# Performance work log

Hardware: AMD Instinct MI355X
Metric: run time of the kernel (lower is better)

The kernel has to match this reference:

```python
import jax, jax.numpy as jnp
import numpy as np

NUM_EMBEDDINGS = 512
EMBEDDING_DIM = 128
COMMITMENT = 0.25
DECAY = 0.99
EPS = 1e-05


def setup_inputs() -> dict:
    key = jax.random.key(0)
    k1, k2 = jax.random.split(key)
    z = jax.random.normal(k1, (32, EMBEDDING_DIM, 64, 64), dtype=jnp.float32)
    embedding = jax.random.normal(k2, (EMBEDDING_DIM, NUM_EMBEDDINGS), dtype=jnp.float32)
    cluster_size = jnp.zeros((NUM_EMBEDDINGS,), dtype=jnp.float32)
    embed_avg = embedding  # buffer initialized as a clone of embedding
    return {"z": z, "embedding": embedding, "cluster_size": cluster_size, "embed_avg": embed_avg}


def reference(z, embedding, cluster_size, embed_avg):
    sg = jax.lax.stop_gradient
    D, K = embedding.shape
    B, C, H, W = z.shape
    z_perm = jnp.transpose(z, (0, 2, 3, 1))          # [B,H,W,D]
    flat_z = z_perm.reshape(-1, D)                    # [N,D]

    distances = ((flat_z ** 2).sum(1, keepdims=True)
                 - 2.0 * (flat_z @ embedding)
                 + (embedding ** 2).sum(0)[None, :])  # [N,K]
    idx = jnp.argmin(distances, axis=1)               # [N]

    # gather codes (equivalent to one-hot @ embedding.T, without materializing one-hot)
    quantized = jnp.take(embedding.T, idx, axis=0).reshape(z_perm.shape)  # [B,H,W,D]
    quantized = jnp.transpose(quantized, (0, 3, 1, 2))                    # [B,D,H,W]

    # EMA codebook update (training branch)
    enc_sum = jax.ops.segment_sum(jnp.ones_like(idx, dtype=flat_z.dtype), idx, num_segments=K)  # [K]
    embed_sum = jax.ops.segment_sum(flat_z, idx, num_segments=K).T                              # [D,K]
    new_cluster_size = cluster_size * DECAY + (1.0 - DECAY) * enc_sum
    new_embed_avg = embed_avg * DECAY + (1.0 - DECAY) * embed_sum
    n = jnp.maximum(new_cluster_size.sum(), 1e-05)
    cs = (new_cluster_size + EPS) / (n + K * EPS) * n
    new_embedding = new_embed_avg / cs[None, :]

    e_latent_loss = jnp.mean((sg(quantized) - z) ** 2)
    q_latent_loss = jnp.mean((quantized - sg(z)) ** 2)
    loss = q_latent_loss + COMMITMENT * e_latent_loss

    quantized_out = z + sg(quantized - z)             # straight-through
    encoding_indices = idx.reshape(B, H, W)
    return (quantized_out, loss, encoding_indices, new_embedding, new_cluster_size, new_embed_avg)
```

## Files before the change

### kernel.cpp

```cpp
#include <hip/hip_runtime.h>
#include <hip/hip_bf16.h>
#include <float.h>

typedef _Float16 f16;
typedef __attribute__((ext_vector_type(8))) _Float16 half8;
typedef __attribute__((ext_vector_type(4))) float floatx4;

#define DIM   128
#define HW    4096
#define NPOS  131072
#define K     512
#define ZSTRIDE_B 524288

#define Q_OFF     0
#define LOSS_OFF  16777216
#define IDX_OFF   16777217
#define NEMB_OFF  16908289
#define NCS_OFF   16973825
#define NEA_OFF   16974337

#define WS_LOSS  0
#define WS_E2    2
#define WS_ENC   514
#define WS_ESUM  1026
#define WS_ZERO_COUNT 66562
#define WS_EHI   66564
#define WS_ELO   99332

#define XST 136

__global__ __launch_bounds__(256) void k_prep(const float* __restrict__ emb,
                                              f16* __restrict__ ehiP,
                                              f16* __restrict__ eloP,
                                              float* __restrict__ e2) {
    int lin = blockIdx.x * 256 + threadIdx.x;
    int o = lin >> 9, k = lin & 511;
    int g = k >> 4, r = k & 15;
    half8 hh, ll;
    float s = 0.f;
    #pragma unroll
    for (int j = 0; j < 8; ++j) {
        float v = emb[(o * 8 + j) * K + k];
        f16 h = (f16)v;
        f16 l = (f16)(v - (float)h);
        hh[j] = h; ll[j] = l;
        s = fmaf(v, v, s);
    }
    int base = (g * 4 + (o >> 2)) * 512 + (o & 3) * 128 + r * 8;
    *(half8*)&ehiP[base] = hh;
    *(half8*)&eloP[base] = ll;
    unsafeAtomicAdd(&e2[k], s);
}

__global__ __launch_bounds__(256, 2) void k_assign(const float* __restrict__ z,
                                                   const f16* __restrict__ ehiP,
                                                   const f16* __restrict__ eloP,
                                                   const float* __restrict__ e2,
                                                   float* __restrict__ out,
                                                   float* __restrict__ lossAcc) {
    __shared__ f16 xs_h[64 * XST];
    __shared__ f16 xs_l[64 * XST];
    __shared__ float wbD[256];
    __shared__ int   wbI[256];
    __shared__ int   bidx[64];
    __shared__ float wred[4];

    const int tid  = threadIdx.x;
    const int lane = tid & 63;
    const int wv   = tid >> 6;
    const int n0   = blockIdx.x * 64;
    const int b    = n0 >> 12;
    const int hw0  = n0 & 4095;
    const float* zb = z + b * ZSTRIDE_B + hw0;
    const int l15  = lane & 15;
    const int quad = lane >> 4;

    float sv0[16], sv1[16];
    #pragma unroll
    for (int it = 0; it < 16; ++it) {
        int lin = tid + it * 256;
        int i  = lin & 63;
        int dp = lin >> 6;
        sv0[it] = zb[(2 * dp) * HW + i];
        sv1[it] = zb[(2 * dp + 1) * HW + i];
    }
    #pragma unroll
    for (int it = 0; it < 16; ++it) {
        int lin = tid + it * 256;
        int i  = lin & 63;
        int dp = lin >> 6;
        float v0 = sv0[it], v1 = sv1[it];
        f16 h0 = (f16)v0; f16 l0 = (f16)(v0 - (float)h0);
        f16 h1 = (f16)v1; f16 l1 = (f16)(v1 - (float)h1);
        union { f16 h[2]; unsigned int u; } ph, pl;
        ph.h[0] = h0; ph.h[1] = h1;
        pl.h[0] = l0; pl.h[1] = l1;
        *(unsigned int*)&xs_h[i * XST + 2 * dp] = ph.u;
        *(unsigned int*)&xs_l[i * XST + 2 * dp] = pl.u;
    }
    __syncthreads();

    float bestD[4][4];
    int   bestI[4][4];
    #pragma unroll
    for (int t = 0; t < 4; ++t)
        #pragma unroll
        for (int r = 0; r < 4; ++r) { bestD[t][r] = FLT_MAX; bestI[t][r] = 0x7fffffff; }

    const half8* gh = (const half8*)ehiP;
    const half8* gl = (const half8*)eloP;

    for (int cc = 0; cc < 4; ++cc) {
        floatx4 acc[4][2];
        #pragma unroll
        for (int t = 0; t < 4; ++t)
            #pragma unroll
            for (int nt = 0; nt < 2; ++nt) acc[t][nt] = (floatx4){0.f, 0.f, 0.f, 0.f};

        for (int dc = 0; dc < 4; ++dc) {
            half8 ah[4], al[4];
            #pragma unroll
            for (int t = 0; t < 4; ++t) {
                int off = (t * 16 + l15) * XST + dc * 32 + quad * 8;
                ah[t] = *(const half8*)&xs_h[off];
                al[t] = *(const half8*)&xs_l[off];
            }
            #pragma unroll
            for (int nt = 0; nt < 2; ++nt) {
                int g  = cc * 8 + wv * 2 + nt;
                int bi = (g * 4 + dc) * 64 + lane;
                half8 bh = gh[bi];
                half8 bl = gl[bi];
                #pragma unroll
                for (int t = 0; t < 4; ++t) {
                    acc[t][nt] = __builtin_amdgcn_mfma_f32_16x16x32_f16(ah[t], bh, acc[t][nt], 0, 0, 0);
                    acc[t][nt] = __builtin_amdgcn_mfma_f32_16x16x32_f16(al[t], bh, acc[t][nt], 0, 0, 0);
                    acc[t][nt] = __builtin_amdgcn_mfma_f32_16x16x32_f16(ah[t], bl, acc[t][nt], 0, 0, 0);
                }
            }
        }
        #pragma unroll
        for (int nt = 0; nt < 2; ++nt) {
            int c = cc * 128 + wv * 32 + nt * 16 + l15;
            float ee = e2[c];
            #pragma unroll
            for (int t = 0; t < 4; ++t)
                #pragma unroll
                for (int r = 0; r < 4; ++r) {
                    float s = fmaf(-2.f, acc[t][nt][r], ee);
                    if (s < bestD[t][r]) { bestD[t][r] = s; bestI[t][r] = c; }
                }
        }
    }

    #pragma unroll
    for (int mask = 1; mask <= 8; mask <<= 1) {
        #pragma unroll
        for (int t = 0; t < 4; ++t)
            #pragma unroll
            for (int r = 0; r < 4; ++r) {
                float od = __shfl_xor(bestD[t][r], mask, 64);
                int   oi = __shfl_xor(bestI[t][r], mask, 64);
                if (od < bestD[t][r] || (od == bestD[t][r] && oi < bestI[t][r])) {
                    bestD[t][r] = od; bestI[t][r] = oi;
                }
            }
    }
    if (l15 == 0) {
        #pragma unroll
        for (int t = 0; t < 4; ++t)
            #pragma unroll
            for (int r = 0; r < 4; ++r) {
                int m = t * 16 + quad * 4 + r;
                wbD[wv * 64 + m] = bestD[t][r];
                wbI[wv * 64 + m] = bestI[t][r];
            }
    }
    __syncthreads();
    if (tid < 64) {
        float bd = wbD[tid]; int bi = wbI[tid];
        #pragma unroll
        for (int w = 1; w < 4; ++w) {
            float od = wbD[w * 64 + tid]; int oi = wbI[w * 64 + tid];
            if (od < bd || (od == bd && oi < bi)) { bd = od; bi = oi; }
        }
        bidx[tid] = bi;
        out[IDX_OFF + n0 + tid] = (float)bi;
    }
    __syncthreads();

    float* qb = out + Q_OFF + b * ZSTRIDE_B + hw0;
    float lsum = 0.f;
    #pragma unroll
    for (int it = 0; it < 4; ++it) {
        int o = wv * 4 + it;
        int c = bidx[lane];
        int g = c >> 4, r = c & 15;
        int base = (g * 4 + (o >> 2)) * 512 + (o & 3) * 128 + r * 8;
        half8 hh = *(const half8*)&ehiP[base];
        half8 ll = *(const half8*)&eloP[base];
        half8 zh = *(const half8*)&xs_h[lane * XST + o * 8];
        half8 zl = *(const half8*)&xs_l[lane * XST + o * 8];
        #pragma unroll
        for (int jj = 0; jj < 8; ++jj) {
            float q  = (float)hh[jj] + (float)ll[jj];
            float zz = (float)zh[jj] + (float)zl[jj];
            qb[(o * 8 + jj) * HW + lane] = q;
            float df = q - zz;
            lsum = fmaf(df, df, lsum);
        }
    }
    #pragma unroll
    for (int m = 32; m >= 1; m >>= 1) lsum += __shfl_xor(lsum, m, 64);
    if (lane == 0) wred[wv] = lsum;
    __syncthreads();
    if (tid == 0) unsafeAtomicAdd(lossAcc, wred[0] + wred[1] + wred[2] + wred[3]);
}

#define DC 8
__global__ __launch_bounds__(256) void k_ema2(const float* __restrict__ z,
                                              const float* __restrict__ out,
                                              float* __restrict__ enc,
                                              float* __restrict__ esum) {
    __shared__ float acc[DC][K];
    __shared__ float cnt[K];

    const int tid = threadIdx.x;
    const int half   = blockIdx.x & 1;
    const int dchunk = (blockIdx.x >> 1) & 15;
    const int b      = blockIdx.x >> 5;
    const int d0 = dchunk * DC;
    const bool doCnt = (dchunk == 0);

    for (int i = tid; i < DC * K; i += 256) ((float*)acc)[i] = 0.f;
    if (doCnt) for (int i = tid; i < K; i += 256) cnt[i] = 0.f;
    __syncthreads();

    const float* zb  = z + b * ZSTRIDE_B;
    const float* idp = out + IDX_OFF + b * HW;

    const int p0 = half * 2048;
    for (int t = p0; t < p0 + 2048; t += 1024) {
        const int p = t + 4 * tid;
        float4 iv = *(const float4*)(idp + p);
        int k0 = (int)iv.x;
        int k1 = (int)iv.y;
        int k2 = (int)iv.z;
        int k3 = (int)iv.w;
        if (doCnt) {
            atomicAdd(&cnt[k0], 1.f); atomicAdd(&cnt[k1], 1.f);
            atomicAdd(&cnt[k2], 1.f); atomicAdd(&cnt[k3], 1.f);
        }
        #pragma unroll
        for (int d = 0; d < DC; ++d) {
            float4 zv = *(const float4*)(zb + (d0 + d) * HW + p);
            atomicAdd(&acc[d][k0], zv.x);
            atomicAdd(&acc[d][k1], zv.y);
            atomicAdd(&acc[d][k2], zv.z);
            atomicAdd(&acc[d][k3], zv.w);
        }
    }
    __syncthreads();

    const int rot = (blockIdx.x & 31) << 6;
    for (int i = tid; i < DC * K; i += 256) {
        int j = (i + rot) & (DC * K - 1);
        int d = j >> 9, k = j & 511;
        unsafeAtomicAdd(&esum[(d0 + d) * K + k], acc[d][k]);
    }
    if (doCnt) for (int i = tid; i < K; i += 256) unsafeAtomicAdd(&enc[i], cnt[i]);
}

__global__ __launch_bounds__(512) void k_final(const float* __restrict__ enc,
                                               const float* __restrict__ cs_in,
                                               const float* __restrict__ lossAcc,
                                               const float* __restrict__ esum,
                                               const float* __restrict__ eavg_in,
                                               float* __restrict__ out) {
    __shared__ float red[512];
    int k = threadIdx.x;
    int d = blockIdx.x;
    float ncs = fmaf(cs_in[k], 0.99f, 0.01f * enc[k]);
    red[k] = ncs;
    __syncthreads();
    for (int s = 256; s > 0; s >>= 1) {
        if (k < s) red[k] += red[k + s];
        __syncthreads();
    }
    float nn = fmaxf(red[0], 1e-5f);
    float cs = (ncs + 1e-5f) / (nn + (float)K * 1e-5f) * nn;
    float ea = fmaf(eavg_in[d * K + k], 0.99f, 0.01f * esum[d * K + k]);
    out[NEA_OFF + d * K + k] = ea;
    out[NEMB_OFF + d * K + k] = ea / cs;
    if (d == 0) {
        out[NCS_OFF + k] = ncs;
        if (k == 0) out[LOSS_OFF] = lossAcc[0] * 1.25f / 16777216.0f;
    }
}

extern "C" void kernel_launch(void* const* d_in, const int* in_sizes, int n_in,
                              void* d_out, int out_size, void* d_ws, size_t ws_size,
                              hipStream_t stream) {
    const float* z     = (const float*)d_in[0];
    const float* emb   = (const float*)d_in[1];
    const float* cs_in = (const float*)d_in[2];
    const float* eavg  = (const float*)d_in[3];
    float* out = (float*)d_out;
    float* wsF = (float*)d_ws;

    hipMemsetAsync(wsF, 0, WS_ZERO_COUNT * sizeof(float), stream);

    k_prep<<<32, 256, 0, stream>>>(emb, (f16*)(wsF + WS_EHI), (f16*)(wsF + WS_ELO),
                                   wsF + WS_E2);
    k_assign<<<NPOS / 64, 256, 0, stream>>>(z,
                                            (const f16*)(wsF + WS_EHI),
                                            (const f16*)(wsF + WS_ELO),
                                            wsF + WS_E2, out, wsF + WS_LOSS);
    k_ema2<<<1024, 256, 0, stream>>>(z, out, wsF + WS_ENC, wsF + WS_ESUM);
    k_final<<<128, 512, 0, stream>>>(wsF + WS_ENC, cs_in, wsF + WS_LOSS,
                                     wsF + WS_ESUM, eavg, out);
}
```

Before: 301.2 us.

## Move quantized output write and loss into EMA scatter kernel

```diff
diff --git a/kernel.cpp b/kernel.cpp
--- a/kernel.cpp
+++ b/kernel.cpp
@@ -56,14 +56,11 @@
                                                    const f16* __restrict__ ehiP,
                                                    const f16* __restrict__ eloP,
                                                    const float* __restrict__ e2,
-                                                   float* __restrict__ out,
-                                                   float* __restrict__ lossAcc) {
+                                                   float* __restrict__ out) {
     __shared__ f16 xs_h[64 * XST];
     __shared__ f16 xs_l[64 * XST];
     __shared__ float wbD[256];
     __shared__ int   wbI[256];
-    __shared__ int   bidx[64];
-    __shared__ float wred[4];
 
     const int tid  = threadIdx.x;
     const int lane = tid & 63;
@@ -184,60 +181,42 @@
             float od = wbD[w * 64 + tid]; int oi = wbI[w * 64 + tid];
             if (od < bd || (od == bd && oi < bi)) { bd = od; bi = oi; }
         }
-        bidx[tid] = bi;
         out[IDX_OFF + n0 + tid] = (float)bi;
     }
-    __syncthreads();
-
-    float* qb = out + Q_OFF + b * ZSTRIDE_B + hw0;
-    float lsum = 0.f;
-    #pragma unroll
-    for (int it = 0; it < 4; ++it) {
-        int o = wv * 4 + it;
-        int c = bidx[lane];
-        int g = c >> 4, r = c & 15;
-        int base = (g * 4 + (o >> 2)) * 512 + (o & 3) * 128 + r * 8;
-        half8 hh = *(const half8*)&ehiP[base];
-        half8 ll = *(const half8*)&eloP[base];
-        half8 zh = *(const half8*)&xs_h[lane * XST + o * 8];
-        half8 zl = *(const half8*)&xs_l[lane * XST + o * 8];
-        #pragma unroll
-        for (int jj = 0; jj < 8; ++jj) {
-            float q  = (float)hh[jj] + (float)ll[jj];
-            float zz = (float)zh[jj] + (float)zl[jj];
-            qb[(o * 8 + jj) * HW + lane] = q;
-            float df = q - zz;
-            lsum = fmaf(df, df, lsum);
-        }
-    }
-    #pragma unroll
-    for (int m = 32; m >= 1; m >>= 1) lsum += __shfl_xor(lsum, m, 64);
-    if (lane == 0) wred[wv] = lsum;
-    __syncthreads();
-    if (tid == 0) unsafeAtomicAdd(lossAcc, wred[0] + wred[1] + wred[2] + wred[3]);
 }
 
 #define DC 8
 __global__ __launch_bounds__(256) void k_ema2(const float* __restrict__ z,
-                                              const float* __restrict__ out,
+                                              const float* __restrict__ emb,
+                                              float* __restrict__ out,
                                               float* __restrict__ enc,
-                                              float* __restrict__ esum) {
+                                              float* __restrict__ esum,
+                                              float* __restrict__ lossAcc) {
     __shared__ float acc[DC][K];
+    __shared__ float embs[DC][K];
     __shared__ float cnt[K];
+    __shared__ float wred[4];
 
     const int tid = threadIdx.x;
+    const int lane = tid & 63;
+    const int wv = tid >> 6;
     const int half   = blockIdx.x & 1;
     const int dchunk = (blockIdx.x >> 1) & 15;
     const int b      = blockIdx.x >> 5;
     const int d0 = dchunk * DC;
     const bool doCnt = (dchunk == 0);
 
-    for (int i = tid; i < DC * K; i += 256) ((float*)acc)[i] = 0.f;
+    for (int i = tid; i < DC * K; i += 256) {
+        ((float*)acc)[i] = 0.f;
+        ((float*)embs)[i] = emb[d0 * K + i];
+    }
     if (doCnt) for (int i = tid; i < K; i += 256) cnt[i] = 0.f;
     __syncthreads();
 
     const float* zb  = z + b * ZSTRIDE_B;
     const float* idp = out + IDX_OFF + b * HW;
+    float* qb = out + Q_OFF + b * ZSTRIDE_B;
+    float lsum = 0.f;
 
     const int p0 = half * 2048;
     for (int t = p0; t < p0 + 2048; t += 1024) {
@@ -258,9 +237,22 @@
             atomicAdd(&acc[d][k1], zv.y);
             atomicAdd(&acc[d][k2], zv.z);
             atomicAdd(&acc[d][k3], zv.w);
-        }
-    }
-    __syncthreads();
+            float4 qv;
+            qv.x = embs[d][k0]; qv.y = embs[d][k1];
+            qv.z = embs[d][k2]; qv.w = embs[d][k3];
+            *(float4*)(qb + (d0 + d) * HW + p) = qv;
+            float dx = qv.x - zv.x; lsum = fmaf(dx, dx, lsum);
+            float dy = qv.y - zv.y; lsum = fmaf(dy, dy, lsum);
+            float dz2 = qv.z - zv.z; lsum = fmaf(dz2, dz2, lsum);
+            float dw = qv.w - zv.w; lsum = fmaf(dw, dw, lsum);
+        }
+    }
+
+    #pragma unroll
+    for (int m = 32; m >= 1; m >>= 1) lsum += __shfl_xor(lsum, m, 64);
+    if (lane == 0) wred[wv] = lsum;
+    __syncthreads();
+    if (tid == 0) unsafeAtomicAdd(lossAcc, wred[0] + wred[1] + wred[2] + wred[3]);
 
     const int rot = (blockIdx.x & 31) << 6;
     for (int i = tid; i < DC * K; i += 256) {
@@ -315,8 +307,9 @@
     k_assign<<<NPOS / 64, 256, 0, stream>>>(z,
                                             (const f16*)(wsF + WS_EHI),
                                             (const f16*)(wsF + WS_ELO),
-                                            wsF + WS_E2, out, wsF + WS_LOSS);
-    k_ema2<<<1024, 256, 0, stream>>>(z, out, wsF + WS_ENC, wsF + WS_ESUM);
+                                            wsF + WS_E2, out);
+    k_ema2<<<1024, 256, 0, stream>>>(z, emb, out, wsF + WS_ENC, wsF + WS_ESUM,
+                                     wsF + WS_LOSS);
     k_final<<<128, 512, 0, stream>>>(wsF + WS_ENC, cs_in, wsF + WS_LOSS,
                                      wsF + WS_ESUM, eavg, out);
 }
```

Result: faster. 283.5 us (-5.9%).
